# Performance work log

Measured on AMD Instinct MI355X. Metric: run time of the kernel, lower is better.

## Reference

```python
import jax, jax.numpy as jnp
import numpy as np

TEMP = 0.07  # InfoCNECauchy temperature


def setup_inputs() -> dict:
    key = jax.random.key(0)
    k1, k2 = jax.random.split(key)
    features = jax.random.normal(k1, (8192, 512), dtype=jnp.float32)  # 2N x d, two augmented views
    labels = jax.random.randint(k2, (8192,), 0, 100)  # unused in selfsupervised mode
    return {"features": features, "labels": labels}


def reference(features, labels):
    n2 = features.shape[0]
    n = n2 // 2
    # squared pairwise Euclidean distances (== torch.cdist(...)**2)
    sq = jnp.sum(features * features, axis=1)
    d2 = jnp.maximum(sq[:, None] + sq[None, :] - 2.0 * (features @ features.T), 0.0)
    # Cauchy similarity kernel: 1 / ((dist / t)^2 + 1)
    sim = 1.0 / (d2 / (TEMP * TEMP) + 1.0)
    # selfsupervised mask: row i is positive only with its partner view i^N,
    # so the masked mean-log reduces to log(sim[i, partner(i)])
    idx = jnp.arange(n2)
    partner = jnp.where(idx < n, idx + n, idx - n)
    pos = jnp.mean(jnp.log(sim[idx, partner]))
    # negatives: sum over row excluding the diagonal (sim diag == 1)
    neg = jnp.mean(jnp.log(jnp.sum(sim, axis=1) - jnp.diagonal(sim)))
    return -(pos - neg)
```

## Files before the change

### kernel.cpp

```cpp
#include <hip/hip_runtime.h>


#define N2 8192
#define DIM 512
#define NT 64
#define NTILES (NT * (NT + 1) / 2)
#define T2 0.0049f

typedef float floatx4 __attribute__((ext_vector_type(4)));
typedef __bf16 bf16x8 __attribute__((ext_vector_type(8)));
typedef __bf16 bf16x4 __attribute__((ext_vector_type(4)));

__device__ __forceinline__ void load_to_lds16(const void* g, void* l) {
  auto gp = (const __attribute__((address_space(1))) void*)(reinterpret_cast<uintptr_t>(g));
  auto lp = (__attribute__((address_space(3))) void*)(reinterpret_cast<uintptr_t>(l));
  __builtin_amdgcn_global_load_lds(gp, lp, 16, 0, 0);
}

__global__ __launch_bounds__(256) void prep_kernel(const float* __restrict__ f,
                                                   __bf16* __restrict__ fbf,
                                                   float* __restrict__ sq,
                                                   float* __restrict__ rowsum) {
  const int t = threadIdx.x;
  if (t < 2) rowsum[blockIdx.x * 2 + t] = 0.f;
  const int row = blockIdx.x * 2 + (t >> 7);
  const int ci = (t & 127) * 4;
  const float4 v = *(const float4*)(f + (size_t)row * DIM + ci);
  bf16x4 b;
  b[0] = (__bf16)v.x; b[1] = (__bf16)v.y; b[2] = (__bf16)v.z; b[3] = (__bf16)v.w;
  *(bf16x4*)(fbf + (size_t)row * DIM + ci) = b;
  float s = v.x * v.x + v.y * v.y + v.z * v.z + v.w * v.w;
#pragma unroll
  for (int off = 1; off < 64; off <<= 1) s += __shfl_xor(s, off, 64);
  __shared__ float red[4];
  if ((t & 63) == 0) red[t >> 6] = s;
  __syncthreads();
  if ((t & 127) == 0) sq[row] = red[t >> 6] + red[(t >> 6) + 1];
}

__global__ __launch_bounds__(256) void gemm_kernel(const __bf16* __restrict__ fbf,
                                                   const float* __restrict__ sq,
                                                   float* __restrict__ rowsum,
                                                   float* __restrict__ spart) {
  __shared__ __bf16 aT[128 * 32];
  __shared__ __bf16 bT[128 * 32];

  {
    const int x = blockIdx.x & 7;
    int kk = blockIdx.x >> 3;
    int band = x;
    const int n1 = 250 - 16 * x;
    if (kk >= n1) { kk -= n1; band = 15 - x; }
    const int by0 = band * 4;
    int bxx = by0;
    int cnt;
    while (kk >= (cnt = min(4, bxx - by0 + 1))) { kk -= cnt; ++bxx; }
    __shared__ int s_by, s_bx;
    if (threadIdx.x == 0) { s_by = by0 + kk; s_bx = bxx; }
    __syncthreads();
    (void)s_by;
  }
  int by, bx;
  {
    const int x = blockIdx.x & 7;
    int kk = blockIdx.x >> 3;
    int band = x;
    const int n1 = 250 - 16 * x;
    if (kk >= n1) { kk -= n1; band = 15 - x; }
    const int by0 = band * 4;
    int bxx = by0;
    int cnt;
    while (kk >= (cnt = min(4, bxx - by0 + 1))) { kk -= cnt; ++bxx; }
    by = by0 + kk;
    bx = bxx;
  }
  const int brow = by * 128;
  const int bcol = bx * 128;
  const bool diag = (by == bx);

  const int t = threadIdx.x;
  const int lane = t & 63;
  const int w = t >> 6;
  const int wrow = (w >> 1) * 64;
  const int wcol = (w & 1) * 64;
  const int q4 = lane >> 4;
  const int lc = lane & 15;

  floatx4 acc[4][4] = {};

  int grow[2], gofs[2];
#pragma unroll
  for (int it = 0; it < 2; ++it) {
    const int slot = it * 256 + t;
    const int rp = slot >> 3;
    const int u = (slot & 7) ^ (rp & 7);
    grow[it] = rp * 2 + (u >> 2);
    gofs[it] = (u & 3) * 8;
  }

  const int up = (((lc & 1) * 4) + q4) ^ (lc >> 1);
  const int rhalf = lc >> 1;

  for (int kt = 0; kt < DIM / 32; ++kt) {
    const int k0 = kt * 32;
#pragma unroll
    for (int it = 0; it < 2; ++it) {
      load_to_lds16(fbf + (size_t)(brow + grow[it]) * DIM + k0 + gofs[it],
                    &aT[t * 8 + it * 2048]);
      load_to_lds16(fbf + (size_t)(bcol + grow[it]) * DIM + k0 + gofs[it],
                    &bT[t * 8 + it * 2048]);
    }
    __syncthreads();
    bf16x8 af[4], bfr[4];
#pragma unroll
    for (int mr = 0; mr < 4; ++mr)
      af[mr] = *(const bf16x8*)&aT[((wrow >> 1) + mr * 8 + rhalf) * 64 + up * 8];
#pragma unroll
    for (int mc = 0; mc < 4; ++mc)
      bfr[mc] = *(const bf16x8*)&bT[((wcol >> 1) + mc * 8 + rhalf) * 64 + up * 8];
#pragma unroll
    for (int mr = 0; mr < 4; ++mr)
#pragma unroll
      for (int mc = 0; mc < 4; ++mc)
        acc[mr][mc] =
            __builtin_amdgcn_mfma_f32_16x16x32_bf16(af[mr], bfr[mc], acc[mr][mc], 0, 0, 0);
    __syncthreads();
  }

  float sqc[4];
#pragma unroll
  for (int mc = 0; mc < 4; ++mc) sqc[mc] = sq[bcol + wcol + mc * 16 + lc];

  float cs[4] = {0.f, 0.f, 0.f, 0.f};

#pragma unroll
  for (int mr = 0; mr < 4; ++mr) {
#pragma unroll
    for (int reg = 0; reg < 4; ++reg) {
      const int r = brow + wrow + mr * 16 + q4 * 4 + reg;
      const float sr = sq[r];
      const int pc = r ^ (N2 / 2);
      float rs = 0.f;
#pragma unroll
      for (int mc = 0; mc < 4; ++mc) {
        const int c = bcol + wcol + mc * 16 + lc;
        const float g = acc[mr][mc][reg];
        const float d2 = fmaxf(sr + sqc[mc] - 2.f * g, 0.f);
        const float s = T2 * __builtin_amdgcn_rcpf(d2 + T2);
        if (c != r) rs += s;
        cs[mc] += s;
        if (c == pc) { spart[r] = s; spart[pc] = s; }
      }
#pragma unroll
      for (int off = 1; off < 16; off <<= 1) rs += __shfl_xor(rs, off, 64);
      if (lc == 0) atomicAdd(&rowsum[r], rs);
    }
  }

  if (!diag) {
#pragma unroll
    for (int mc = 0; mc < 4; ++mc) {
      float v = cs[mc];
      v += __shfl_xor(v, 16, 64);
      v += __shfl_xor(v, 32, 64);
      if (lane < 16) atomicAdd(&rowsum[bcol + wcol + mc * 16 + lane], v);
    }
  }
}

__global__ __launch_bounds__(256) void final_kernel(const float* __restrict__ rowsum,
                                                    const float* __restrict__ spart,
                                                    float* __restrict__ out) {
  const int t = threadIdx.x;
  float a = 0.f;
  for (int r = t; r < N2; r += 256) a += logf(rowsum[r]) - logf(spart[r]);
#pragma unroll
  for (int off = 1; off < 64; off <<= 1) a += __shfl_xor(a, off, 64);
  __shared__ float red[4];
  if ((t & 63) == 0) red[t >> 6] = a;
  __syncthreads();
  if (t == 0) out[0] = (red[0] + red[1] + red[2] + red[3]) * (1.0f / (float)N2);
}

extern "C" void kernel_launch(void* const* d_in, const int* in_sizes, int n_in,
                              void* d_out, int out_size, void* d_ws, size_t ws_size,
                              hipStream_t stream) {
  const float* features = (const float*)d_in[0];
  float* out = (float*)d_out;

  char* ws = (char*)d_ws;
  __bf16* fbf = (__bf16*)ws;
  float* sq = (float*)(ws + (size_t)N2 * DIM * sizeof(__bf16));
  float* rowsum = sq + N2;
  float* spart = rowsum + N2;

  prep_kernel<<<N2 / 2, 256, 0, stream>>>(features, fbf, sq, rowsum);
  gemm_kernel<<<NTILES, 256, 0, stream>>>(fbf, sq, rowsum, spart);
  final_kernel<<<1, 256, 0, stream>>>(rowsum, spart, out);
}
```

Baseline: 142.8 us.

## Use 256x256 tiles with 8-wave ping-pong pipelined MFMA schedule

```diff
diff --git a/kernel.cpp b/kernel.cpp
--- a/kernel.cpp
+++ b/kernel.cpp
@@ -3,8 +3,8 @@
 
 #define N2 8192
 #define DIM 512
-#define NT 64
-#define NTILES (NT * (NT + 1) / 2)
+#define TNT 32
+#define NTILES 528
 #define T2 0.0049f
 
 typedef float floatx4 __attribute__((ext_vector_type(4)));
@@ -38,133 +38,181 @@
   if ((t & 127) == 0) sq[row] = red[t >> 6] + red[(t >> 6) + 1];
 }
 
-__global__ __launch_bounds__(256) void gemm_kernel(const __bf16* __restrict__ fbf,
-                                                   const float* __restrict__ sq,
-                                                   float* __restrict__ rowsum,
-                                                   float* __restrict__ spart) {
-  __shared__ __bf16 aT[128 * 32];
-  __shared__ __bf16 bT[128 * 32];
-
-  {
-    const int x = blockIdx.x & 7;
-    int kk = blockIdx.x >> 3;
-    int band = x;
-    const int n1 = 250 - 16 * x;
-    if (kk >= n1) { kk -= n1; band = 15 - x; }
-    const int by0 = band * 4;
-    int bxx = by0;
-    int cnt;
-    while (kk >= (cnt = min(4, bxx - by0 + 1))) { kk -= cnt; ++bxx; }
-    __shared__ int s_by, s_bx;
-    if (threadIdx.x == 0) { s_by = by0 + kk; s_bx = bxx; }
-    __syncthreads();
-    (void)s_by;
-  }
+#define LDSREG(op, d, h, ks) (((((op)*2 + (d))*2 + (h))*2 + (ks)) * 4096)
+#define SB __builtin_amdgcn_sched_barrier(0)
+#define PHASE_MID do { SB; __builtin_amdgcn_s_barrier(); SB; } while (0)
+#define PHASE_END do { SB; __builtin_amdgcn_s_barrier(); SB; } while (0)
+#define VM4 asm volatile("s_waitcnt vmcnt(4)" ::: "memory")
+#define VM0 asm volatile("s_waitcnt vmcnt(0)" ::: "memory")
+
+__global__ __launch_bounds__(512, 2) void gemm_kernel(const __bf16* __restrict__ fbf,
+                                                      const float* __restrict__ sq,
+                                                      float* __restrict__ rowsum,
+                                                      float* __restrict__ spart) {
+  __shared__ __bf16 lds[16 * 4096];
+
   int by, bx;
   {
     const int x = blockIdx.x & 7;
     int kk = blockIdx.x >> 3;
     int band = x;
-    const int n1 = 250 - 16 * x;
+    const int n1 = 63 - 4 * x;
     if (kk >= n1) { kk -= n1; band = 15 - x; }
-    const int by0 = band * 4;
+    const int by0 = band * 2;
     int bxx = by0;
     int cnt;
-    while (kk >= (cnt = min(4, bxx - by0 + 1))) { kk -= cnt; ++bxx; }
+    while (kk >= (cnt = min(2, bxx - by0 + 1))) { kk -= cnt; ++bxx; }
     by = by0 + kk;
     bx = bxx;
   }
-  const int brow = by * 128;
-  const int bcol = bx * 128;
+  const int brow = by * 256;
+  const int bcol = bx * 256;
   const bool diag = (by == bx);
+  const bool ptile = (bx == by + 16);
 
   const int t = threadIdx.x;
   const int lane = t & 63;
   const int w = t >> 6;
-  const int wrow = (w >> 1) * 64;
-  const int wcol = (w & 1) * 64;
+  const int wr = w >> 2;
+  const int wc = w & 3;
   const int q4 = lane >> 4;
   const int lc = lane & 15;
-
-  floatx4 acc[4][4] = {};
-
-  int grow[2], gofs[2];
-#pragma unroll
-  for (int it = 0; it < 2; ++it) {
-    const int slot = it * 256 + t;
-    const int rp = slot >> 3;
-    const int u = (slot & 7) ^ (rp & 7);
-    grow[it] = rp * 2 + (u >> 2);
-    gofs[it] = (u & 3) * 8;
-  }
-
-  const int up = (((lc & 1) * 4) + q4) ^ (lc >> 1);
   const int rhalf = lc >> 1;
-
-  for (int kt = 0; kt < DIM / 32; ++kt) {
-    const int k0 = kt * 32;
-#pragma unroll
-    for (int it = 0; it < 2; ++it) {
-      load_to_lds16(fbf + (size_t)(brow + grow[it]) * DIM + k0 + gofs[it],
-                    &aT[t * 8 + it * 2048]);
-      load_to_lds16(fbf + (size_t)(bcol + grow[it]) * DIM + k0 + gofs[it],
-                    &bT[t * 8 + it * 2048]);
+  const int up = (((lc & 1) * 4) + q4) ^ rhalf;
+
+  const int rp = t >> 3;
+  const int uu = (t & 7) ^ (rp & 7);
+  const int grow = rp * 2 + (uu >> 2);
+  const int gofs = (uu & 3) * 8;
+
+  floatx4 acc[4][4][2] = {};
+  bf16x8 af[4][2];
+  bf16x8 bv0[2][2], bv1[2][2];
+
+#define STAGE(kt, opB, h) do {                                                \
+    const int kt_ = (kt);                                                     \
+    const int dd_ = kt_ & 1;                                                  \
+    const size_t srow_ = (size_t)(((opB) ? bcol : brow) + (h)*128 + grow);    \
+    load_to_lds16(fbf + srow_ * DIM + kt_ * 64 + gofs,                        \
+                  &lds[LDSREG((opB), dd_, (h), 0) + t * 8]);                  \
+    load_to_lds16(fbf + srow_ * DIM + kt_ * 64 + 32 + gofs,                   \
+                  &lds[LDSREG((opB), dd_, (h), 1) + t * 8]);                  \
+  } while (0)
+
+#define READ_A(d, qm) do {                                                    \
+    _Pragma("unroll") for (int mf = 0; mf < 4; ++mf)                          \
+      _Pragma("unroll") for (int ks = 0; ks < 2; ++ks)                        \
+        af[mf][ks] = *(const bf16x8*)&lds[LDSREG(0, d, qm, ks) +              \
+            (wr * 32 + mf * 8 + rhalf) * 64 + up * 8];                        \
+  } while (0)
+
+#define READ_B(d, qn, BV) do {                                                \
+    _Pragma("unroll") for (int nf = 0; nf < 2; ++nf)                          \
+      _Pragma("unroll") for (int ks = 0; ks < 2; ++ks)                        \
+        BV[nf][ks] = *(const bf16x8*)&lds[LDSREG(1, d, qn, ks) +              \
+            (wc * 16 + nf * 8 + rhalf) * 64 + up * 8];                        \
+  } while (0)
+
+#define MFMAS(qid, BV) do {                                                   \
+    __builtin_amdgcn_s_setprio(1);                                           \
+    _Pragma("unroll") for (int mf = 0; mf < 4; ++mf)                          \
+      _Pragma("unroll") for (int nf = 0; nf < 2; ++nf)                        \
+        _Pragma("unroll") for (int ks = 0; ks < 2; ++ks)                      \
+          acc[qid][mf][nf] = __builtin_amdgcn_mfma_f32_16x16x32_bf16(         \
+              af[mf][ks], BV[nf][ks], acc[qid][mf][nf], 0, 0, 0);             \
+    __builtin_amdgcn_s_setprio(0);                                            \
+  } while (0)
+
+  STAGE(0, 0, 0); STAGE(0, 0, 1); STAGE(0, 1, 0); STAGE(0, 1, 1);
+  STAGE(1, 0, 0); STAGE(1, 1, 0);
+  VM4;
+  PHASE_MID;
+
+#pragma unroll 1
+  for (int k2 = 0; k2 < 6; k2 += 2) {
+    READ_A(0, 0); READ_B(0, 0, bv0); STAGE(k2 + 1, 0, 1);
+    PHASE_MID; MFMAS(0, bv0); PHASE_END;
+    READ_B(0, 1, bv1);                STAGE(k2 + 1, 1, 1);
+    PHASE_MID; MFMAS(1, bv1); PHASE_END;
+    READ_A(0, 1);                     STAGE(k2 + 2, 0, 0);
+    PHASE_MID; MFMAS(2, bv0); PHASE_END;
+                                      STAGE(k2 + 2, 1, 0);
+    PHASE_MID; MFMAS(3, bv1); VM4; PHASE_END;
+    READ_A(1, 0); READ_B(1, 0, bv0);  STAGE(k2 + 2, 0, 1);
+    PHASE_MID; MFMAS(0, bv0); PHASE_END;
+    READ_B(1, 1, bv1);                STAGE(k2 + 2, 1, 1);
+    PHASE_MID; MFMAS(1, bv1); PHASE_END;
+    READ_A(1, 1);                     STAGE(k2 + 3, 0, 0);
+    PHASE_MID; MFMAS(2, bv0); PHASE_END;
+                                      STAGE(k2 + 3, 1, 0);
+    PHASE_MID; MFMAS(3, bv1); VM4; PHASE_END;
+  }
+
+  READ_A(0, 0); READ_B(0, 0, bv0); STAGE(7, 0, 1);
+  PHASE_MID; MFMAS(0, bv0); PHASE_END;
+  READ_B(0, 1, bv1);               STAGE(7, 1, 1);
+  PHASE_MID; MFMAS(1, bv1); PHASE_END;
+  READ_A(0, 1);
+  PHASE_MID; MFMAS(2, bv0); PHASE_END;
+  PHASE_MID; MFMAS(3, bv1); VM0; PHASE_END;
+  READ_A(1, 0); READ_B(1, 0, bv0);
+  PHASE_MID; MFMAS(0, bv0); PHASE_END;
+  READ_B(1, 1, bv1);
+  PHASE_MID; MFMAS(1, bv1); PHASE_END;
+  READ_A(1, 1);
+  PHASE_MID; MFMAS(2, bv0); PHASE_END;
+  PHASE_MID; MFMAS(3, bv1); PHASE_END;
+
+  asm volatile("" ::: "memory");
+
+  float sqc[2][2];
+#pragma unroll
+  for (int qn = 0; qn < 2; ++qn)
+#pragma unroll
+    for (int nf = 0; nf < 2; ++nf)
+      sqc[qn][nf] = sq[bcol + qn * 128 + wc * 32 + nf * 16 + lc] + T2;
+
+  float cs[2][2] = {{0.f, 0.f}, {0.f, 0.f}};
+
+#pragma unroll
+  for (int qm = 0; qm < 2; ++qm) {
+#pragma unroll
+    for (int mf = 0; mf < 4; ++mf) {
+#pragma unroll
+      for (int reg = 0; reg < 4; ++reg) {
+        const int r = brow + qm * 128 + wr * 64 + mf * 16 + q4 * 4 + reg;
+        const float sr = sq[r];
+        const int pc = r ^ (N2 / 2);
+        float rs = 0.f;
+#pragma unroll
+        for (int qn = 0; qn < 2; ++qn) {
+#pragma unroll
+          for (int nf = 0; nf < 2; ++nf) {
+            const int c = bcol + qn * 128 + wc * 32 + nf * 16 + lc;
+            const float g = acc[qm * 2 + qn][mf][nf][reg];
+            const float u = __builtin_amdgcn_rcpf(fmaxf(sr + sqc[qn][nf] - 2.f * g, T2));
+            if (c != r) rs += u;
+            cs[qn][nf] += u;
+            if (ptile && c == pc) { const float s = T2 * u; spart[r] = s; spart[pc] = s; }
+          }
+        }
+#pragma unroll
+        for (int off = 1; off < 16; off <<= 1) rs += __shfl_xor(rs, off, 64);
+        if (lc == 0) atomicAdd(&rowsum[r], T2 * rs);
+      }
     }
-    __syncthreads();
-    bf16x8 af[4], bfr[4];
-#pragma unroll
-    for (int mr = 0; mr < 4; ++mr)
-      af[mr] = *(const bf16x8*)&aT[((wrow >> 1) + mr * 8 + rhalf) * 64 + up * 8];
-#pragma unroll
-    for (int mc = 0; mc < 4; ++mc)
-      bfr[mc] = *(const bf16x8*)&bT[((wcol >> 1) + mc * 8 + rhalf) * 64 + up * 8];
-#pragma unroll
-    for (int mr = 0; mr < 4; ++mr)
-#pragma unroll
-      for (int mc = 0; mc < 4; ++mc)
-        acc[mr][mc] =
-            __builtin_amdgcn_mfma_f32_16x16x32_bf16(af[mr], bfr[mc], acc[mr][mc], 0, 0, 0);
-    __syncthreads();
-  }
-
-  float sqc[4];
-#pragma unroll
-  for (int mc = 0; mc < 4; ++mc) sqc[mc] = sq[bcol + wcol + mc * 16 + lc];
-
-  float cs[4] = {0.f, 0.f, 0.f, 0.f};
-
-#pragma unroll
-  for (int mr = 0; mr < 4; ++mr) {
-#pragma unroll
-    for (int reg = 0; reg < 4; ++reg) {
-      const int r = brow + wrow + mr * 16 + q4 * 4 + reg;
-      const float sr = sq[r];
-      const int pc = r ^ (N2 / 2);
-      float rs = 0.f;
-#pragma unroll
-      for (int mc = 0; mc < 4; ++mc) {
-        const int c = bcol + wcol + mc * 16 + lc;
-        const float g = acc[mr][mc][reg];
-        const float d2 = fmaxf(sr + sqc[mc] - 2.f * g, 0.f);
-        const float s = T2 * __builtin_amdgcn_rcpf(d2 + T2);
-        if (c != r) rs += s;
-        cs[mc] += s;
-        if (c == pc) { spart[r] = s; spart[pc] = s; }
+  }
+
+  if (!diag) {
+#pragma unroll
+    for (int qn = 0; qn < 2; ++qn)
+#pragma unroll
+      for (int nf = 0; nf < 2; ++nf) {
+        float v = cs[qn][nf];
+        v += __shfl_xor(v, 16, 64);
+        v += __shfl_xor(v, 32, 64);
+        if (lane < 16) atomicAdd(&rowsum[bcol + qn * 128 + wc * 32 + nf * 16 + lane], T2 * v);
       }
-#pragma unroll
-      for (int off = 1; off < 16; off <<= 1) rs += __shfl_xor(rs, off, 64);
-      if (lc == 0) atomicAdd(&rowsum[r], rs);
-    }
-  }
-
-  if (!diag) {
-#pragma unroll
-    for (int mc = 0; mc < 4; ++mc) {
-      float v = cs[mc];
-      v += __shfl_xor(v, 16, 64);
-      v += __shfl_xor(v, 32, 64);
-      if (lane < 16) atomicAdd(&rowsum[bcol + wcol + mc * 16 + lane], v);
-    }
   }
 }
 
@@ -195,6 +243,6 @@
   float* spart = rowsum + N2;
 
   prep_kernel<<<N2 / 2, 256, 0, stream>>>(features, fbf, sq, rowsum);
-  gemm_kernel<<<NTILES, 256, 0, stream>>>(fbf, sq, rowsum, spart);
+  gemm_kernel<<<NTILES, 512, 0, stream>>>(fbf, sq, rowsum, spart);
   final_kernel<<<1, 256, 0, stream>>>(rowsum, spart, out);
 }
```

Result: slower. 170.3 us (+19.3%).
